# Kernel optimization log

Hardware: AMD Instinct MI355X
Metric: run time of the kernel (lower is better)

## Reference

```python
import jax, jax.numpy as jnp
import numpy as np

EMBED = 1024
HEADS = 16
HEAD_DIM = EMBED // HEADS
B, S = 4, 2048


def setup_inputs() -> dict:
    key = jax.random.key(0)
    ks = jax.random.split(key, 13)
    scale = 1.0 / np.sqrt(EMBED)
    inp = {
        "query": jax.random.normal(ks[0], (B, S, EMBED), dtype=jnp.float32),
        "key": jax.random.normal(ks[1], (B, S, EMBED), dtype=jnp.float32),
        "value": jax.random.normal(ks[2], (B, S, EMBED), dtype=jnp.float32),
        "mask": jax.random.randint(ks[3], (B, 1, S, S), 0, 2) > 0,
        "Wq": jax.random.normal(ks[4], (EMBED, EMBED), dtype=jnp.float32) * scale,
        "bq": jnp.zeros((EMBED,), dtype=jnp.float32),
        "Wk": jax.random.normal(ks[5], (EMBED, EMBED), dtype=jnp.float32) * scale,
        "bk": jnp.zeros((EMBED,), dtype=jnp.float32),
        "Wv": jax.random.normal(ks[6], (EMBED, EMBED), dtype=jnp.float32) * scale,
        "bv": jnp.zeros((EMBED,), dtype=jnp.float32),
        "Wo": jax.random.normal(ks[7], (EMBED, EMBED), dtype=jnp.float32) * scale,
        "bo": jnp.zeros((EMBED,), dtype=jnp.float32),
    }
    return inp


def _split_heads(x):
    b, s, _ = x.shape
    return x.reshape(b, s, HEADS, HEAD_DIM).transpose(0, 2, 1, 3)  # [B,H,S,Dh]


def reference(query, key, value, mask, Wq, bq, Wk, bk, Wv, bv, Wo, bo):
    # Linear projections (torch Linear: x @ W.T + b)
    q = _split_heads(query @ Wq.T + bq)
    k = _split_heads(key @ Wk.T + bk)
    v = _split_heads(value @ Wv.T + bv)
    # scaled dot-product attention with full score matrix (as in source)
    scores = jnp.einsum("bhqd,bhkd->bhqk", q, k) / jnp.sqrt(jnp.float32(HEAD_DIM))
    scores = jnp.where(mask, jnp.float32(-1e9), scores)
    attn = jax.nn.softmax(scores, axis=-1)  # dropout p=0 -> identity
    out = jnp.einsum("bhqk,bhkd->bhqd", attn, v)
    out = out.transpose(0, 2, 1, 3).reshape(out.shape[0], -1, EMBED)
    return out @ Wo.T + bo
```

## Files before the change

### kernel.cpp

```cpp
#include <hip/hip_runtime.h>
#include <cstdint>

#define B_  4
#define H_  16
#define S_  2048
#define DH_ 64
#define E_  1024
#define M_  (B_ * S_)

typedef __attribute__((ext_vector_type(8))) __bf16 bf16x8;
typedef __attribute__((ext_vector_type(4))) __bf16 bf16x4;
typedef __attribute__((ext_vector_type(4))) float  f32x4;

__device__ __forceinline__ uint16_t f2bf(float f) {
    union { float f; uint32_t u; } v; v.f = f;
    uint32_t u = v.u;
    uint32_t r = (u + 0x7fffu + ((u >> 16) & 1u)) >> 16;
    return (uint16_t)r;
}
__device__ __forceinline__ uint32_t pack2(float a, float b) {
    return (uint32_t)f2bf(a) | ((uint32_t)f2bf(b) << 16);
}

__device__ __forceinline__ uint32_t cvt_pk_bf16(float lo, float hi) {
    uint32_t r;
    asm("v_cvt_pk_bf16_f32 %0, %1, %2" : "=v"(r) : "v"(lo), "v"(hi));
    return r;
}

__device__ __forceinline__ float exp2_fast(float x) {
#if __has_builtin(__builtin_amdgcn_exp2f)
    return __builtin_amdgcn_exp2f(x);
#else
    float r; asm("v_exp_f32 %0, %1" : "=v"(r) : "v"(x)); return r;
#endif
}

__device__ __forceinline__ void glds16(const void* g, void* lds_base) {
    __builtin_amdgcn_global_load_lds(
        (const __attribute__((address_space(1))) uint32_t*)g,
        (__attribute__((address_space(3))) uint32_t*)lds_base, 16, 0, 0);
}

__global__ void prep_kernel(const float* __restrict__ q, const float* __restrict__ k,
                            const float* __restrict__ v,
                            const float* __restrict__ w0, const float* __restrict__ w1,
                            const float* __restrict__ w2, const float* __restrict__ w3,
                            uint16_t* __restrict__ wbf,
                            uint16_t* __restrict__ qa, uint16_t* __restrict__ ka,
                            uint16_t* __restrict__ va) {
    int bid = blockIdx.x;
    const float* src; uint16_t* dst; int base;
    if (bid < 2048) {
        int i = bid * 256 + threadIdx.x;
        base = i * 8;
        int wsel = base >> 20;
        src = (wsel == 0) ? w0 : (wsel == 1) ? w1 : (wsel == 2) ? w2 : w3;
        dst = wbf + base;
        base &= 1048575;
    } else {
        int r = bid - 2048;
        int sel = r >> 12;
        int i = (r & 4095) * 256 + threadIdx.x;
        base = i * 8;
        src = (sel == 0) ? q : (sel == 1) ? k : v;
        dst = ((sel == 0) ? qa : (sel == 1) ? ka : va) + base;
    }
    float4 a = *(const float4*)(src + base);
    float4 b = *(const float4*)(src + base + 4);
    uint4 o;
    o.x = pack2(a.x, a.y); o.y = pack2(a.z, a.w);
    o.z = pack2(b.x, b.y); o.w = pack2(b.z, b.w);
    *(uint4*)dst = o;
}

__global__ void mask_bits_kernel(const int* __restrict__ mask, uint64_t* __restrict__ bits) {
    int idx = blockIdx.x * 256 + threadIdx.x;
    uint64_t b = __ballot(mask[idx] != 0);
    if ((threadIdx.x & 63) == 0) bits[idx >> 6] = b;
}

__global__ __launch_bounds__(256, 2)
void gemm_bt_kernel(const uint16_t* __restrict__ A0, const uint16_t* __restrict__ A1,
                    const uint16_t* __restrict__ A2,
                    const uint16_t* __restrict__ Bw0,
                    const float* __restrict__ bias0, const float* __restrict__ bias1,
                    const float* __restrict__ bias2,
                    void* __restrict__ out0, void* __restrict__ out1,
                    void* __restrict__ out2,
                    int multi) {
    const int z = blockIdx.z;
    const uint16_t* A  = (z == 0) ? A0 : (z == 1) ? A1 : A2;
    const uint16_t* Bw = Bw0 + (size_t)z * 1048576;
    const float* bias  = (z == 0) ? bias0 : (z == 1) ? bias1 : bias2;
    void* out          = (z == 0) ? out0 : (z == 1) ? out1 : out2;
    const float scale  = (multi && z == 0) ? 0.18033688f : 1.0f;
    const int mode     = multi ? ((z == 2) ? 2 : 1) : 0;

    const int m0 = blockIdx.y * 128;
    const int n0 = blockIdx.x * 128;

    __shared__ __align__(16) uint16_t As[128 * 64];
    __shared__ __align__(16) uint16_t Bs[128 * 64];

    const int t    = threadIdx.x;
    const int w    = t >> 6;
    const int lane = t & 63;
    const int ln   = lane & 15;
    const int quad = lane >> 4;
    const int wr   = w >> 1;
    const int wc   = w & 1;

    f32x4 acc[4][4];
    const f32x4 z4 = {0.f, 0.f, 0.f, 0.f};
#pragma unroll
    for (int i = 0; i < 4; ++i)
#pragma unroll
        for (int j = 0; j < 4; ++j) acc[i][j] = z4;

    const char* Ag = (const char*)(A  + (size_t)m0 * E_);
    const char* Bg = (const char*)(Bw + (size_t)n0 * E_);
    const int rsub = lane >> 3;
    const int colb = ((lane & 7) ^ rsub) * 16;

    for (int kk = 0; kk < E_; kk += 64) {
#pragma unroll
        for (int c = 0; c < 4; ++c) {
            glds16(Ag + (size_t)(c * 32 + w * 8 + rsub) * 2048 + kk * 2 + colb,
                   (char*)As + c * 4096 + w * 1024);
            glds16(Bg + (size_t)(c * 32 + w * 8 + rsub) * 2048 + kk * 2 + colb,
                   (char*)Bs + c * 4096 + w * 1024);
        }
        __syncthreads();

#pragma unroll
        for (int ks = 0; ks < 2; ++ks) {
            bf16x8 af[4], bf[4];
#pragma unroll
            for (int mt = 0; mt < 4; ++mt)
                af[mt] = *(const bf16x8*)&As[(wr * 64 + mt * 16 + ln) * 64 +
                                             (((ks * 4 + quad) ^ (ln & 7)) * 8)];
#pragma unroll
            for (int nt = 0; nt < 4; ++nt)
                bf[nt] = *(const bf16x8*)&Bs[(wc * 64 + nt * 16 + ln) * 64 +
                                             (((ks * 4 + quad) ^ (ln & 7)) * 8)];
#pragma unroll
            for (int mt = 0; mt < 4; ++mt)
#pragma unroll
                for (int nt = 0; nt < 4; ++nt)
                    acc[mt][nt] = __builtin_amdgcn_mfma_f32_16x16x32_bf16(
                        af[mt], bf[nt], acc[mt][nt], 0, 0, 0);
        }
        __syncthreads();
    }

#pragma unroll
    for (int mt = 0; mt < 4; ++mt) {
        const int rowb = m0 + wr * 64 + mt * 16 + quad * 4;
#pragma unroll
        for (int nt = 0; nt < 4; ++nt) {
            const int col = n0 + wc * 64 + nt * 16 + ln;
            const float bsum = bias[col];
            if (mode == 2) {
                int bb = rowb >> 11, s0 = rowb & 2047, hh = col >> 6, d = col & 63;
                float v0 = acc[mt][nt][0] + bsum, v1 = acc[mt][nt][1] + bsum;
                float v2 = acc[mt][nt][2] + bsum, v3 = acc[mt][nt][3] + bsum;
                uint2 o; o.x = pack2(v0, v1); o.y = pack2(v2, v3);
                *(uint2*)((uint16_t*)out + (((size_t)bb * H_ + hh) * DH_ + d) * S_ + s0) = o;
            } else {
#pragma unroll
                for (int r = 0; r < 4; ++r) {
                    float vv = (acc[mt][nt][r] + bsum) * scale;
                    int rr = rowb + r;
                    if (mode == 1) {
                        int bb = rr >> 11, s = rr & 2047, hh = col >> 6, d = col & 63;
                        ((uint16_t*)out)[(((size_t)bb * H_ + hh) * S_ + s) * DH_ + d] = f2bf(vv);
                    } else {
                        ((float*)out)[(size_t)rr * E_ + col] = vv;
                    }
                }
            }
        }
    }
}

__global__ __launch_bounds__(256, 2)
void attn_kernel(const uint16_t* __restrict__ qb, const uint16_t* __restrict__ kb,
                 const uint16_t* __restrict__ vtb, const uint32_t* __restrict__ mbits,
                 uint16_t* __restrict__ attn_out) {
    const int wg   = blockIdx.x;
    const int xcd  = wg & 7;
    const int rest = wg >> 3;
    const int qt   = rest & 31;
    const int bh   = ((rest >> 5) << 3) | xcd;
    const int b    = bh >> 4, h = bh & 15;

    __shared__ __align__(16) char smem[51200];
    uint16_t* p_all = (uint16_t*)smem;

    const int t    = threadIdx.x;
    const int w    = t >> 6;
    const int lane = t & 63;
    const int ln   = lane & 15;
    const int quad = lane >> 4;
    const int ln2  = ln << 1;

    const char* qg  = (const char*)(qb  + ((size_t)bh * S_ + qt * 64) * DH_);
    const char* kg  = (const char*)(kb  + (size_t)bh * S_ * DH_);
    const char* vtg = (const char*)(vtb + (size_t)bh * DH_ * S_);

    bf16x8 aq[4][2];
#pragma unroll
    for (int mt = 0; mt < 4; ++mt)
#pragma unroll
        for (int ks = 0; ks < 2; ++ks)
            aq[mt][ks] = *(const bf16x8*)(qg + (size_t)(mt * 16 + ln) * 128 +
                                          ks * 64 + quad * 16);

    f32x4 acc_o[4][4];
    const f32x4 z4 = {0.f, 0.f, 0.f, 0.f};
#pragma unroll
    for (int mt = 0; mt < 4; ++mt)
#pragma unroll
        for (int nt = 0; nt < 4; ++nt) acc_o[mt][nt] = z4;
    float lr[4][4];
#pragma unroll
    for (int mt = 0; mt < 4; ++mt)
#pragma unroll
        for (int r = 0; r < 4; ++r) lr[mt][r] = 0.f;

    uint16_t* pw = p_all + w * 2304;

    const char* kp0 = kg + (size_t)(w * 32 + ln2) * 128 + quad * 16;
    const char* kp1 = kg + (size_t)(w * 32 + ln2 + 1) * 128 + quad * 16;
    const char* vp  = vtg + (size_t)ln * 4096 + w * 64 + quad * 16;
    const char* mp  = (const char*)(mbits + ((size_t)b * S_ + qt * 64) * 64) +
                      (quad * 4) * 256 + w * 4;

    bf16x8 kf[2][2];
#pragma unroll
    for (int ks = 0; ks < 2; ++ks) {
        kf[ks][0] = *(const bf16x8*)(kp0 + ks * 64);
        kf[ks][1] = *(const bf16x8*)(kp1 + ks * 64);
    }

    for (int it = 0; it < 16; ++it) {
        bf16x8 bv[4];
#pragma unroll
        for (int nt = 0; nt < 4; ++nt)
            bv[nt] = *(const bf16x8*)(vp + (size_t)nt * 65536);
        uint32_t mk[4][4];
#pragma unroll
        for (int mt = 0; mt < 4; ++mt)
#pragma unroll
            for (int r = 0; r < 4; ++r)
                mk[mt][r] = *(const uint32_t*)(mp + mt * 4096 + r * 256);
        bf16x8 kn[2][2];
#pragma unroll
        for (int ks = 0; ks < 2; ++ks) {
            kn[ks][0] = *(const bf16x8*)(kp0 + 16384 + ks * 64);
            kn[ks][1] = *(const bf16x8*)(kp1 + 16384 + ks * 64);
        }

        f32x4 sc[4][2];
#pragma unroll
        for (int mt = 0; mt < 4; ++mt) { sc[mt][0] = z4; sc[mt][1] = z4; }
#pragma unroll
        for (int ks = 0; ks < 2; ++ks)
#pragma unroll
            for (int mt = 0; mt < 4; ++mt) {
                sc[mt][0] = __builtin_amdgcn_mfma_f32_16x16x32_bf16(aq[mt][ks], kf[ks][0], sc[mt][0], 0, 0, 0);
                sc[mt][1] = __builtin_amdgcn_mfma_f32_16x16x32_bf16(aq[mt][ks], kf[ks][1], sc[mt][1], 0, 0, 0);
            }

#pragma unroll
        for (int mt = 0; mt < 4; ++mt)
#pragma unroll
            for (int r = 0; r < 4; ++r) {
                uint32_t sh = mk[mt][r] >> ln2;
                float e0 = (sh & 1u) ? 0.f : exp2_fast(sc[mt][0][r]);
                float e1 = (sh & 2u) ? 0.f : exp2_fast(sc[mt][1][r]);
                lr[mt][r] += e0 + e1;
                *(uint32_t*)&pw[(mt * 16 + quad * 4 + r) * 36 + ln2] = cvt_pk_bf16(e0, e1);
            }

#pragma unroll
        for (int mt = 0; mt < 4; ++mt) {
            bf16x4 lo = *(const bf16x4*)&pw[(mt * 16 + ln) * 36 + quad * 8];
            bf16x4 hi = *(const bf16x4*)&pw[(mt * 16 + ln) * 36 + quad * 8 + 4];
            bf16x8 ap = __builtin_shufflevector(lo, hi, 0, 1, 2, 3, 4, 5, 6, 7);
#pragma unroll
            for (int nt = 0; nt < 4; ++nt)
                acc_o[mt][nt] = __builtin_amdgcn_mfma_f32_16x16x32_bf16(ap, bv[nt], acc_o[mt][nt], 0, 0, 0);
        }

#pragma unroll
        for (int ks = 0; ks < 2; ++ks) {
            kf[ks][0] = kn[ks][0];
            kf[ks][1] = kn[ks][1];
        }
        kp0 += 16384; kp1 += 16384; vp += 256; mp += 16;
    }

#pragma unroll
    for (int mt = 0; mt < 4; ++mt)
#pragma unroll
        for (int r = 0; r < 4; ++r) {
            float v = lr[mt][r];
            v += __shfl_xor(v, 1);
            v += __shfl_xor(v, 2);
            v += __shfl_xor(v, 4);
            v += __shfl_xor(v, 8);
            lr[mt][r] = v;
        }

    __syncthreads();
    float* obuf = (float*)smem;
    float* lbuf = (float*)(smem + 49920);

    if (ln == 0) {
#pragma unroll
        for (int mt = 0; mt < 4; ++mt)
#pragma unroll
            for (int r = 0; r < 4; ++r)
                lbuf[w * 64 + mt * 16 + quad * 4 + r] = lr[mt][r];
    }
#pragma unroll
    for (int mt = 0; mt < 4; ++mt) {
        if (mt != w) {
            int ridx = mt * 3 + (w > mt ? w - 1 : w);
            float* reg = obuf + ridx * 1040;
#pragma unroll
            for (int nt = 0; nt < 4; ++nt)
#pragma unroll
                for (int rr = 0; rr < 4; ++rr)
                    reg[(quad * 4 + rr) * 65 + nt * 16 + ln] = acc_o[mt][nt][rr];
        }
    }
    __syncthreads();

    f32x4 accf[4];
#pragma unroll
    for (int nt = 0; nt < 4; ++nt) accf[nt] = acc_o[0][nt];
#pragma unroll
    for (int mt = 1; mt < 4; ++mt)
        if (w == mt) {
#pragma unroll
            for (int nt = 0; nt < 4; ++nt) accf[nt] = acc_o[mt][nt];
        }
#pragma unroll
    for (int widx = 0; widx < 3; ++widx) {
        const float* reg = obuf + (w * 3 + widx) * 1040;
#pragma unroll
        for (int nt = 0; nt < 4; ++nt)
#pragma unroll
            for (int rr = 0; rr < 4; ++rr)
                accf[nt][rr] += reg[(quad * 4 + rr) * 65 + nt * 16 + ln];
    }
    float invl[4];
#pragma unroll
    for (int rr = 0; rr < 4; ++rr) {
        int row = w * 16 + quad * 4 + rr;
        float lt = lbuf[row] + lbuf[64 + row] + lbuf[128 + row] + lbuf[192 + row];
        invl[rr] = 1.0f / lt;
    }
    const size_t orow = (size_t)(b * S_ + qt * 64 + w * 16 + quad * 4);
#pragma unroll
    for (int rr = 0; rr < 4; ++rr)
#pragma unroll
        for (int nt = 0; nt < 4; ++nt)
            attn_out[(orow + rr) * E_ + h * 64 + nt * 16 + ln] = f2bf(accf[nt][rr] * invl[rr]);
}

extern "C" void kernel_launch(void* const* d_in, const int* in_sizes, int n_in,
                              void* d_out, int out_size, void* d_ws, size_t ws_size,
                              hipStream_t stream) {
    const float* query = (const float*)d_in[0];
    const float* key_  = (const float*)d_in[1];
    const float* value = (const float*)d_in[2];
    const int*   mask  = (const int*)d_in[3];
    const float* Wq = (const float*)d_in[4];
    const float* bq = (const float*)d_in[5];
    const float* Wk = (const float*)d_in[6];
    const float* bk = (const float*)d_in[7];
    const float* Wv = (const float*)d_in[8];
    const float* bv = (const float*)d_in[9];
    const float* Wo = (const float*)d_in[10];
    const float* bo = (const float*)d_in[11];

    char* ws = (char*)d_ws;
    uint16_t* wbf   = (uint16_t*)ws;
    uint16_t* qa    = (uint16_t*)(ws + (8u   << 20));
    uint16_t* ka    = (uint16_t*)(ws + (24u  << 20));
    uint16_t* va    = (uint16_t*)(ws + (40u  << 20));
    uint16_t* qproj = (uint16_t*)(ws + (56u  << 20));
    uint16_t* kproj = (uint16_t*)(ws + (72u  << 20));
    uint16_t* vtp   = (uint16_t*)(ws + (88u  << 20));
    uint16_t* atto  = (uint16_t*)(ws + (104u << 20));
    uint64_t* mbits = (uint64_t*)(ws + (120u << 20));

    prep_kernel<<<14336, 256, 0, stream>>>(query, key_, value, Wq, Wk, Wv, Wo,
                                           wbf, qa, ka, va);
    mask_bits_kernel<<<65536, 256, 0, stream>>>(mask, mbits);

    gemm_bt_kernel<<<dim3(E_ / 128, M_ / 128, 3), 256, 0, stream>>>(
        qa, ka, va, wbf, bq, bk, bv, qproj, kproj, vtp, 1);

    attn_kernel<<<dim3(2048), 256, 0, stream>>>(
        qproj, kproj, vtp, (const uint32_t*)mbits, atto);

    gemm_bt_kernel<<<dim3(E_ / 128, M_ / 128, 1), 256, 0, stream>>>(
        atto, atto, atto, wbf + 3145728, bo, bo, bo, d_out, d_out, d_out, 0);
}
```

Before: 468.9 us.

## Permute mask bits for vector loads and shrink attention LDS for occupancy

```diff
diff --git a/kernel.cpp b/kernel.cpp
--- a/kernel.cpp
+++ b/kernel.cpp
@@ -74,10 +74,24 @@
     *(uint4*)dst = o;
 }
 
-__global__ void mask_bits_kernel(const int* __restrict__ mask, uint64_t* __restrict__ bits) {
+__global__ void mask_bits_kernel(const int* __restrict__ mask, uint32_t* __restrict__ bits) {
     int idx = blockIdx.x * 256 + threadIdx.x;
-    uint64_t b = __ballot(mask[idx] != 0);
-    if ((threadIdx.x & 63) == 0) bits[idx >> 6] = b;
+    uint64_t bl = __ballot(mask[idx] != 0);
+    if ((threadIdx.x & 63) == 0) {
+        int col = idx & 2047;
+        int row = (idx >> 11) & 2047;
+        int b   = idx >> 22;
+        int qt = row >> 6, sl = row & 63;
+        int mt = sl >> 4, quad = (sl >> 2) & 3, r = sl & 3;
+        int c0 = col >> 5;
+        int it0 = c0 >> 2, wv0 = c0 & 3;
+        int it1 = (c0 + 1) >> 2, wv1 = (c0 + 1) & 3;
+        size_t bq = (size_t)(b * 32 + qt);
+        size_t i0 = ((((bq * 4 + wv0) * 16 + it0) * 4 + quad) * 4 + mt) * 4 + r;
+        size_t i1 = ((((bq * 4 + wv1) * 16 + it1) * 4 + quad) * 4 + mt) * 4 + r;
+        bits[i0] = (uint32_t)bl;
+        bits[i1] = (uint32_t)(bl >> 32);
+    }
 }
 
 __global__ __launch_bounds__(256, 2)
@@ -184,7 +198,7 @@
     }
 }
 
-__global__ __launch_bounds__(256, 2)
+__global__ __launch_bounds__(256, 4)
 void attn_kernel(const uint16_t* __restrict__ qb, const uint16_t* __restrict__ kb,
                  const uint16_t* __restrict__ vtb, const uint32_t* __restrict__ mbits,
                  uint16_t* __restrict__ attn_out) {
@@ -195,7 +209,7 @@
     const int bh   = ((rest >> 5) << 3) | xcd;
     const int b    = bh >> 4, h = bh & 15;
 
-    __shared__ __align__(16) char smem[51200];
+    __shared__ __align__(16) char smem[19456];
     uint16_t* p_all = (uint16_t*)smem;
 
     const int t    = threadIdx.x;
@@ -234,8 +248,7 @@
     const char* kp0 = kg + (size_t)(w * 32 + ln2) * 128 + quad * 16;
     const char* kp1 = kg + (size_t)(w * 32 + ln2 + 1) * 128 + quad * 16;
     const char* vp  = vtg + (size_t)ln * 4096 + w * 64 + quad * 16;
-    const char* mp  = (const char*)(mbits + ((size_t)b * S_ + qt * 64) * 64) +
-                      (quad * 4) * 256 + w * 4;
+    const uint32_t* mw = mbits + (((size_t)(b * 32 + qt) * 4 + w) << 10);
 
     bf16x8 kf[2][2];
 #pragma unroll
@@ -249,12 +262,10 @@
 #pragma unroll
         for (int nt = 0; nt < 4; ++nt)
             bv[nt] = *(const bf16x8*)(vp + (size_t)nt * 65536);
-        uint32_t mk[4][4];
+        uint4 mk4[4];
 #pragma unroll
         for (int mt = 0; mt < 4; ++mt)
-#pragma unroll
-            for (int r = 0; r < 4; ++r)
-                mk[mt][r] = *(const uint32_t*)(mp + mt * 4096 + r * 256);
+            mk4[mt] = *(const uint4*)(mw + it * 64 + quad * 16 + mt * 4);
         bf16x8 kn[2][2];
 #pragma unroll
         for (int ks = 0; ks < 2; ++ks) {
@@ -274,15 +285,17 @@
             }
 
 #pragma unroll
-        for (int mt = 0; mt < 4; ++mt)
+        for (int mt = 0; mt < 4; ++mt) {
+            const uint32_t* mkp = (const uint32_t*)&mk4[mt];
 #pragma unroll
             for (int r = 0; r < 4; ++r) {
-                uint32_t sh = mk[mt][r] >> ln2;
+                uint32_t sh = mkp[r] >> ln2;
                 float e0 = (sh & 1u) ? 0.f : exp2_fast(sc[mt][0][r]);
                 float e1 = (sh & 2u) ? 0.f : exp2_fast(sc[mt][1][r]);
                 lr[mt][r] += e0 + e1;
                 *(uint32_t*)&pw[(mt * 16 + quad * 4 + r) * 36 + ln2] = cvt_pk_bf16(e0, e1);
             }
+        }
 
 #pragma unroll
         for (int mt = 0; mt < 4; ++mt) {
@@ -299,7 +312,7 @@
             kf[ks][0] = kn[ks][0];
             kf[ks][1] = kn[ks][1];
         }
-        kp0 += 16384; kp1 += 16384; vp += 256; mp += 16;
+        kp0 += 16384; kp1 += 16384; vp += 256;
     }
 
 #pragma unroll
@@ -314,10 +327,8 @@
             lr[mt][r] = v;
         }
 
-    __syncthreads();
     float* obuf = (float*)smem;
-    float* lbuf = (float*)(smem + 49920);
-
+    float* lbuf = (float*)(smem + 18432);
     if (ln == 0) {
 #pragma unroll
         for (int mt = 0; mt < 4; ++mt)
@@ -325,38 +336,8 @@
             for (int r = 0; r < 4; ++r)
                 lbuf[w * 64 + mt * 16 + quad * 4 + r] = lr[mt][r];
     }
-#pragma unroll
-    for (int mt = 0; mt < 4; ++mt) {
-        if (mt != w) {
-            int ridx = mt * 3 + (w > mt ? w - 1 : w);
-            float* reg = obuf + ridx * 1040;
-#pragma unroll
-            for (int nt = 0; nt < 4; ++nt)
-#pragma unroll
-                for (int rr = 0; rr < 4; ++rr)
-                    reg[(quad * 4 + rr) * 65 + nt * 16 + ln] = acc_o[mt][nt][rr];
-        }
-    }
     __syncthreads();
 
-    f32x4 accf[4];
-#pragma unroll
-    for (int nt = 0; nt < 4; ++nt) accf[nt] = acc_o[0][nt];
-#pragma unroll
-    for (int mt = 1; mt < 4; ++mt)
-        if (w == mt) {
-#pragma unroll
-            for (int nt = 0; nt < 4; ++nt) accf[nt] = acc_o[mt][nt];
-        }
-#pragma unroll
-    for (int widx = 0; widx < 3; ++widx) {
-        const float* reg = obuf + (w * 3 + widx) * 1040;
-#pragma unroll
-        for (int nt = 0; nt < 4; ++nt)
-#pragma unroll
-            for (int rr = 0; rr < 4; ++rr)
-                accf[nt][rr] += reg[(quad * 4 + rr) * 65 + nt * 16 + ln];
-    }
     float invl[4];
 #pragma unroll
     for (int rr = 0; rr < 4; ++rr) {
@@ -364,12 +345,37 @@
         float lt = lbuf[row] + lbuf[64 + row] + lbuf[128 + row] + lbuf[192 + row];
         invl[rr] = 1.0f / lt;
     }
+
     const size_t orow = (size_t)(b * S_ + qt * 64 + w * 16 + quad * 4);
 #pragma unroll
-    for (int rr = 0; rr < 4; ++rr)
-#pragma unroll
-        for (int nt = 0; nt < 4; ++nt)
-            attn_out[(orow + rr) * E_ + h * 64 + nt * 16 + ln] = f2bf(accf[nt][rr] * invl[rr]);
+    for (int nt = 0; nt < 4; ++nt) {
+#pragma unroll
+        for (int mt = 0; mt < 4; ++mt) {
+            if (mt != w) {
+                int ridx = mt * 3 + (w > mt ? w - 1 : w);
+                float* reg = obuf + ridx * 272;
+#pragma unroll
+                for (int rr = 0; rr < 4; ++rr)
+                    reg[(quad * 4 + rr) * 17 + ln] = acc_o[mt][nt][rr];
+            }
+        }
+        __syncthreads();
+        f32x4 af = acc_o[0][nt];
+        if (w == 1) af = acc_o[1][nt];
+        else if (w == 2) af = acc_o[2][nt];
+        else if (w == 3) af = acc_o[3][nt];
+#pragma unroll
+        for (int widx = 0; widx < 3; ++widx) {
+            const float* reg = obuf + (w * 3 + widx) * 272;
+#pragma unroll
+            for (int rr = 0; rr < 4; ++rr)
+                af[rr] += reg[(quad * 4 + rr) * 17 + ln];
+        }
+#pragma unroll
+        for (int rr = 0; rr < 4; ++rr)
+            attn_out[(orow + rr) * E_ + h * 64 + nt * 16 + ln] = f2bf(af[rr] * invl[rr]);
+        if (nt != 3) __syncthreads();
+    }
 }
 
 extern "C" void kernel_launch(void* const* d_in, const int* in_sizes, int n_in,
@@ -397,7 +403,7 @@
     uint16_t* kproj = (uint16_t*)(ws + (72u  << 20));
     uint16_t* vtp   = (uint16_t*)(ws + (88u  << 20));
     uint16_t* atto  = (uint16_t*)(ws + (104u << 20));
-    uint64_t* mbits = (uint64_t*)(ws + (120u << 20));
+    uint32_t* mbits = (uint32_t*)(ws + (120u << 20));
 
     prep_kernel<<<14336, 256, 0, stream>>>(query, key_, value, Wq, Wk, Wv, Wo,
                                            wbf, qa, ka, va);
@@ -407,7 +413,7 @@
         qa, ka, va, wbf, bq, bk, bv, qproj, kproj, vtp, 1);
 
     attn_kernel<<<dim3(2048), 256, 0, stream>>>(
-        qproj, kproj, vtp, (const uint32_t*)mbits, atto);
+        qproj, kproj, vtp, mbits, atto);
 
     gemm_bt_kernel<<<dim3(E_ / 128, M_ / 128, 1), 256, 0, stream>>>(
         atto, atto, atto, wbf + 3145728, bo, bo, bo, d_out, d_out, d_out, 0);
```

After: 809.4 us. 72.6% more time.
